# Kernel tuning notes

Measured on AMD Instinct MI355X. Metric: run time of the kernel, lower is better.

## Reference

```python
import jax, jax.numpy as jnp
import numpy as np


def _conv(x, w, b, pad):
    o = jax.lax.conv_general_dilated(x, w, (1, 1), [(pad, pad), (pad, pad)],
                                     dimension_numbers=('NCHW', 'OIHW', 'NCHW'))
    return o + b[None, :, None, None]


def _prelu(x, a):
    return jnp.where(x >= 0, x, a * x)


def _bn(x, g, b):
    # training-mode BatchNorm2d (biased variance, eps=1e-5)
    m = jnp.mean(x, axis=(0, 2, 3), keepdims=True)
    v = jnp.var(x, axis=(0, 2, 3), keepdims=True)
    return (x - m) * jax.lax.rsqrt(v + 1e-5) * g[None, :, None, None] + b[None, :, None, None]


def _maxpool2(x):
    return jax.lax.reduce_window(x, -jnp.inf, jax.lax.max, (1, 1, 2, 2), (1, 1, 2, 2), 'VALID')


def _up2(x):
    # bilinear upsample x2, align_corners=True
    B, C, H, W = x.shape
    Ho, Wo = 2 * H, 2 * W
    ys = jnp.arange(Ho, dtype=x.dtype) * ((H - 1) / (Ho - 1))
    xs = jnp.arange(Wo, dtype=x.dtype) * ((W - 1) / (Wo - 1))
    y0 = jnp.floor(ys).astype(jnp.int32)
    y1 = jnp.minimum(y0 + 1, H - 1)
    wy = (ys - y0.astype(x.dtype))[:, None]
    x0 = jnp.floor(xs).astype(jnp.int32)
    x1 = jnp.minimum(x0 + 1, W - 1)
    wx = xs - x0.astype(x.dtype)
    rows = x[:, :, y0, :] * (1 - wy) + x[:, :, y1, :] * wy  # [B,C,Ho,W]
    return rows[:, :, :, x0] * (1 - wx) + rows[:, :, :, x1] * wx


def _dyn_conv(x, w):
    # per-sample dynamic conv: x [B,1,H,W], w [B,Cout,k,k], pad = k//2 - 1
    # fused as a single grouped conv (groups = B) instead of B*Cout tiny launches
    B, Cout, k, _ = w.shape
    pad = k // 2 - 1
    xi = x.reshape(1, B, x.shape[2], x.shape[3])
    wi = w.reshape(B * Cout, 1, k, k)
    o = jax.lax.conv_general_dilated(xi, wi, (1, 1), [(pad, pad), (pad, pad)],
                                     dimension_numbers=('NCHW', 'OIHW', 'NCHW'),
                                     feature_group_count=B)
    return o.reshape(B, Cout, o.shape[2], o.shape[3])


def _double(x, w1, b1, w2, b2, a1, a2):
    return _prelu(_conv(_prelu(_conv(x, w1, b1, 1), a1), w2, b2, 1), a2)


def _forward(x, w, c1_w, c1_b, d2_w1, d2_b1, d2_w2, d2_b2, d3_w1, d3_b1, d3_w2, d3_b2,
             d4_w1, d4_b1, d4_w2, d4_b2, u3_w1, u3_b1, u3_w2, u3_b2, u2_w1, u2_b1,
             u2_w2, u2_b2, u1_w1, u1_b1, u1_w2, u1_b2, last_w, last_b,
             bn1_g, bn1_b, bn2_g, bn2_b, bn3_g, bn3_b, bn4_g, bn4_b, prelu_a):
    c1 = _prelu(_dyn_conv(x, w), prelu_a[0])          # [B,32,H-1,W-1]
    c1 = _prelu(_conv(c1, c1_w, c1_b, 2), prelu_a[1])  # 4x4 pad 2 -> [B,32,H,W]
    c1 = _bn(c1, bn1_g, bn1_b)
    h = _maxpool2(c1)
    c2 = _bn(_double(h, d2_w1, d2_b1, d2_w2, d2_b2, prelu_a[2], prelu_a[3]), bn2_g, bn2_b)
    h = _maxpool2(c2)
    c3 = _bn(_double(h, d3_w1, d3_b1, d3_w2, d3_b2, prelu_a[4], prelu_a[5]), bn3_g, bn3_b)
    h = _maxpool2(c3)
    h = _bn(_double(h, d4_w1, d4_b1, d4_w2, d4_b2, prelu_a[6], prelu_a[7]), bn4_g, bn4_b)
    h = jnp.concatenate([_up2(h), c3], axis=1)  # 512+256
    h = _double(h, u3_w1, u3_b1, u3_w2, u3_b2, prelu_a[8], prelu_a[9])
    h = jnp.concatenate([_up2(h), c2], axis=1)  # 256+128
    h = _double(h, u2_w1, u2_b1, u2_w2, u2_b2, prelu_a[10], prelu_a[11])
    h = jnp.concatenate([_up2(h), c1], axis=1)  # 128+32
    h = _double(h, u1_w1, u1_b1, u1_w2, u1_b2, prelu_a[12], prelu_a[13])
    return _conv(h, last_w, last_b, 0)


def setup_inputs() -> dict:
    key = jax.random.key(0)
    ks = iter(jax.random.split(key, 32))
    d = {}
    d['x'] = jax.random.normal(next(ks), (8, 1, 256, 256), jnp.float32)
    d['w'] = jax.random.normal(next(ks), (8, 32, 8, 8), jnp.float32) * 0.1
    wspecs = [('c1_w', (32, 32, 4, 4)), ('d2_w1', (128, 32, 3, 3)), ('d2_w2', (128, 128, 3, 3)),
              ('d3_w1', (256, 128, 3, 3)), ('d3_w2', (256, 256, 3, 3)),
              ('d4_w1', (512, 256, 3, 3)), ('d4_w2', (512, 512, 3, 3)),
              ('u3_w1', (256, 768, 3, 3)), ('u3_w2', (256, 256, 3, 3)),
              ('u2_w1', (128, 384, 3, 3)), ('u2_w2', (128, 128, 3, 3)),
              ('u1_w1', (32, 160, 3, 3)), ('u1_w2', (32, 32, 3, 3)), ('last_w', (1, 32, 1, 1))]
    for name, shp in wspecs:
        d[name] = jax.random.normal(next(ks), shp, jnp.float32) * 0.05
        d[name.replace('_w', '_b')] = jnp.zeros((shp[0],), jnp.float32)
    for name, c in [('bn1', 32), ('bn2', 128), ('bn3', 256), ('bn4', 512)]:
        d[name + '_g'] = jnp.ones((c,), jnp.float32)
        d[name + '_b'] = jnp.zeros((c,), jnp.float32)
    d['prelu_a'] = jnp.full((14,), 0.25, jnp.float32)
    return d


def reference(x, w, c1_w, c1_b, d2_w1, d2_b1, d2_w2, d2_b2, d3_w1, d3_b1, d3_w2, d3_b2,
              d4_w1, d4_b1, d4_w2, d4_b2, u3_w1, u3_b1, u3_w2, u3_b2, u2_w1, u2_b1,
              u2_w2, u2_b2, u1_w1, u1_b1, u1_w2, u1_b2, last_w, last_b,
              bn1_g, bn1_b, bn2_g, bn2_b, bn3_g, bn3_b, bn4_g, bn4_b, prelu_a):
    return _forward(x, w, c1_w, c1_b, d2_w1, d2_b1, d2_w2, d2_b2, d3_w1, d3_b1,
                    d3_w2, d3_b2, d4_w1, d4_b1, d4_w2, d4_b2, u3_w1, u3_b1, u3_w2,
                    u3_b2, u2_w1, u2_b1, u2_w2, u2_b2, u1_w1, u1_b1, u1_w2, u1_b2,
                    last_w, last_b, bn1_g, bn1_b, bn2_g, bn2_b, bn3_g, bn3_b,
                    bn4_g, bn4_b, prelu_a)
```

## Files before the change

kernel.cpp:

```cpp
#include <hip/hip_runtime.h>
#include <hip/hip_bf16.h>
#include <cstddef>


typedef _Float16 h16;
typedef __attribute__((ext_vector_type(8))) _Float16 h16x8;
typedef __attribute__((ext_vector_type(4))) float f32x4;
union F8 { uint4 u; h16x8 h; };
union UH { unsigned u; h16 h[2]; };

__device__ __forceinline__ float h2f(unsigned short s) {
    union { h16 h; unsigned short s; } c; c.s = s; return (float)c.h;
}
__device__ __forceinline__ unsigned short f2h(float f) {
    union { h16 h; unsigned short s; } c; c.h = (h16)f; return c.s;
}
__device__ __forceinline__ unsigned pack2(float a, float b) {
    return (unsigned)f2h(a) | ((unsigned)f2h(b) << 16);
}
__device__ __forceinline__ void up8(const uint4& v, float* f) {
    f[0]=h2f(v.x&0xffff); f[1]=h2f(v.x>>16);
    f[2]=h2f(v.y&0xffff); f[3]=h2f(v.y>>16);
    f[4]=h2f(v.z&0xffff); f[5]=h2f(v.z>>16);
    f[6]=h2f(v.w&0xffff); f[7]=h2f(v.w>>16);
}

__global__ void k_pack(const float* __restrict__ w, h16* __restrict__ pw,
                       int I, int T, int OB)
{
    int i8 = blockIdx.x * 64 + threadIdx.x;
    if (i8 >= (I >> 3)) return;
    int t = blockIdx.y, o = blockIdx.z;
    int ob = o / OB, om = o - ob * OB;
    int mt = om >> 4, m16 = om & 15;
    int chunk = i8 >> 2, quad = i8 & 3;
    int lane = quad * 16 + m16;
    int nch = I >> 5;
    size_t grp = ((((size_t)ob * T + t) * nch + chunk) * (OB >> 4) + mt) * 64 + lane;
    const float* src = w + ((size_t)o * I + i8 * 8) * T + t;
    h16* d = pw + grp * 8;
#pragma unroll
    for (int j = 0; j < 8; ++j) d[j] = (h16)src[(size_t)j * T];
}

template<int KH, int KW, int PAD, bool UPS, int MT>
__global__ __launch_bounds__(256, 2) void k_conv_mfma(
    const h16* __restrict__ src1, int C1n, int H1, int W1,
    const h16* __restrict__ src2, int C2n,
    int Hin, int Win, int Ho, int Wo,
    const h16* __restrict__ PW, const float* __restrict__ bias,
    const float* __restrict__ pa, int aidx,
    h16* __restrict__ out, int Cout)
{
    constexpr int WINH = 8 + KH - 1, WINW = 32 + KW - 1;
    constexpr int NPIX = WINH * WINW;
    constexpr int NIT  = NPIX * 4;
    constexpr int MAXIT = (NIT + 255) / 256;
    constexpr int TAPS = KH * KW;
    __shared__ unsigned short lds[2][NPIX * 36];

    const int tid = threadIdx.x;
    const int lane = tid & 63, wv = tid >> 6;
    const int quad = lane >> 4, m16 = lane & 15;
    const int nCb = Cout / (16 * MT);
    const int b  = blockIdx.z / nCb, cb = blockIdx.z % nCb;
    const int x0 = blockIdx.x * 32, y0 = blockIdx.y * 8;
    const int Cin = C1n + C2n;
    const int nch = Cin >> 5;
    const int co_base = cb * (16 * MT);
    const int srcH = UPS ? Hin : H1;
    const int srcW = UPS ? Win : W1;

    int lof[MAXIT];
    int g1[MAXIT];
    int fl[MAXIT];
    unsigned fyfx[MAXIT];
    int g2[MAXIT];

    const float ry = UPS ? (float)(H1 - 1) / (float)(Hin - 1) : 0.f;
    const float rx = UPS ? (float)(W1 - 1) / (float)(Win - 1) : 0.f;
    const int W1C = UPS ? W1 * C1n : 0;

#pragma unroll
    for (int it = 0; it < MAXIT; ++it) {
        int i = tid + it * 256;
        if (i >= NIT) { lof[it] = -1; g1[it] = -1; g2[it] = -1; fl[it] = 0; fyfx[it] = 0; continue; }
        int p = i >> 2, q = i & 3;
        int wy = p / WINW, wx = p - wy * WINW;
        int yy = y0 - PAD + wy, xx = x0 - PAD + wx;
        lof[it] = p * 36 + q * 8;
        bool val = (unsigned)yy < (unsigned)srcH && (unsigned)xx < (unsigned)srcW;
        if (UPS) {
            fl[it] = 0; fyfx[it] = 0; g1[it] = -1; g2[it] = -1;
            if (val) {
                float ys = yy * ry, xs = xx * rx;
                int yl0 = (int)ys, xl0 = (int)xs;
                float fy = ys - (float)yl0, fx = xs - (float)xl0;
                g1[it] = ((b * H1 + yl0) * W1 + xl0) * C1n + q * 8;
                fl[it] = (yl0 < H1 - 1 ? 1 : 0) | (xl0 < W1 - 1 ? 2 : 0);
                fyfx[it] = pack2(fy, fx);
                g2[it] = ((b * Hin + yy) * Win + xx) * C2n + q * 8;
            }
        } else {
            fl[it] = 0; fyfx[it] = 0; g2[it] = -1;
            g1[it] = val ? ((b * H1 + yy) * W1 + xx) * C1n + q * 8 : -1;
        }
    }

    f32x4 acc[MT][4];
#pragma unroll
    for (int i = 0; i < MT; ++i)
#pragma unroll
        for (int j = 0; j < 4; ++j) acc[i][j] = (f32x4){0.f, 0.f, 0.f, 0.f};

    auto stage = [&](int c0, unsigned short* buf) {
        if (UPS && c0 < C1n) {
#pragma unroll
            for (int it = 0; it < MAXIT; ++it) {
                int lo = lof[it];
                if (lo < 0) continue;
                uint2 lo8 = {0u, 0u}, hi8 = {0u, 0u};
                int g = g1[it];
                if (g >= 0) {
                    const h16* p00 = src1 + g + c0;
                    int oy = (fl[it] & 1) ? W1C : 0;
                    int ox = (fl[it] & 2) ? C1n : 0;
                    F8 v00, v01, v10, v11;
                    v00.u = *(const uint4*)(p00);
                    v01.u = *(const uint4*)(p00 + ox);
                    v10.u = *(const uint4*)(p00 + oy);
                    v11.u = *(const uint4*)(p00 + oy + ox);
                    UH t; t.u = fyfx[it];
                    h16 fy = t.h[0], fx = t.h[1];
                    h16x8 r0 = v00.h + (v10.h - v00.h) * fy;
                    h16x8 r1 = v01.h + (v11.h - v01.h) * fy;
                    F8 rr; rr.h = r0 + (r1 - r0) * fx;
                    lo8 = make_uint2(rr.u.x, rr.u.y);
                    hi8 = make_uint2(rr.u.z, rr.u.w);
                }
                *(uint2*)&buf[lo] = lo8;
                *(uint2*)&buf[lo + 4] = hi8;
            }
        } else if (UPS) {
            int cs = c0 - C1n;
#pragma unroll
            for (int it = 0; it < MAXIT; ++it) {
                int lo = lof[it];
                if (lo < 0) continue;
                uint4 v = {0u, 0u, 0u, 0u};
                int g = g2[it];
                if (g >= 0) v = *(const uint4*)(src2 + g + cs);
                *(uint2*)&buf[lo] = make_uint2(v.x, v.y);
                *(uint2*)&buf[lo + 4] = make_uint2(v.z, v.w);
            }
        } else {
#pragma unroll
            for (int it = 0; it < MAXIT; ++it) {
                int lo = lof[it];
                if (lo < 0) continue;
                uint4 v = {0u, 0u, 0u, 0u};
                int g = g1[it];
                if (g >= 0) v = *(const uint4*)(src1 + g + c0);
                *(uint2*)&buf[lo] = make_uint2(v.x, v.y);
                *(uint2*)&buf[lo + 4] = make_uint2(v.z, v.w);
            }
        }
    };

    const uint4* PW4 = (const uint4*)PW;
    auto sweep = [&](int ci, const unsigned short* buf) {
        size_t abase = (((size_t)cb * TAPS) * nch + ci) * (MT * 64) + lane;
        const size_t astep = (size_t)nch * (MT * 64);
#pragma unroll
        for (int ky = 0; ky < KH; ++ky) {
#pragma unroll
            for (int kx = 0; kx < KW; ++kx) {
                const int tap = ky * KW + kx;
                F8 a[MT];
#pragma unroll
                for (int mt = 0; mt < MT; ++mt)
                    a[mt].u = PW4[abase + (size_t)tap * astep + mt * 64];
#pragma unroll
                for (int nt = 0; nt < 4; ++nt) {
                    int rowl = (wv << 1) + (nt >> 1);
                    int col  = ((nt & 1) << 4) + m16;
                    int li = ((rowl + ky) * WINW + col + kx) * 36 + quad * 8;
                    F8 bf;
                    ((uint2*)&bf)[0] = *(const uint2*)&buf[li];
                    ((uint2*)&bf)[1] = *(const uint2*)&buf[li + 4];
#pragma unroll
                    for (int mt = 0; mt < MT; ++mt)
                        acc[mt][nt] = __builtin_amdgcn_mfma_f32_16x16x32_f16(
                            a[mt].h, bf.h, acc[mt][nt], 0, 0, 0);
                }
            }
        }
    };

    stage(0, lds[0]);
    __syncthreads();
    for (int ci = 0; ci < nch; ++ci) {
        int p = ci & 1;
        if (ci + 1 < nch) stage((ci + 1) << 5, lds[p ^ 1]);
        sweep(ci, lds[p]);
        __syncthreads();
    }

    const float alpha = pa[aidx];
#pragma unroll
    for (int mt = 0; mt < MT; ++mt) {
        int co = co_base + mt * 16 + quad * 4;
        float4 bi = *(const float4*)(bias + co);
#pragma unroll
        for (int nt = 0; nt < 4; ++nt) {
            int y = y0 + (wv << 1) + (nt >> 1);
            int x = x0 + ((nt & 1) << 4) + m16;
            float v0 = acc[mt][nt][0] + bi.x;
            float v1 = acc[mt][nt][1] + bi.y;
            float v2 = acc[mt][nt][2] + bi.z;
            float v3 = acc[mt][nt][3] + bi.w;
            v0 = v0 >= 0.f ? v0 : alpha * v0;
            v1 = v1 >= 0.f ? v1 : alpha * v1;
            v2 = v2 >= 0.f ? v2 : alpha * v2;
            v3 = v3 >= 0.f ? v3 : alpha * v3;
            uint2 r; r.x = pack2(v0, v1); r.y = pack2(v2, v3);
            *(uint2*)(out + ((size_t)((b * Ho + y) * Wo + x)) * Cout + co) = r;
        }
    }
}

__global__ __launch_bounds__(256) void k_dynconv(
    const float* __restrict__ x,
    const float* __restrict__ w,
    const float* __restrict__ pa,
    h16* __restrict__ out)
{
    __shared__ float wl[2048];
    int b = blockIdx.y;
    for (int j = threadIdx.x; j < 2048; j += 256) {
        int t = j >> 5, co = j & 31;
        wl[j] = w[((size_t)(b * 32 + co)) * 64 + t];
    }
    __syncthreads();
    int idx = blockIdx.x * 256 + threadIdx.x;
    if (idx >= 65025) return;
    int py = idx / 255, px = idx - py * 255;
    float acc[32];
#pragma unroll
    for (int c = 0; c < 32; ++c) acc[c] = 0.f;
    const float* xp = x + (size_t)b * 65536;
#pragma unroll
    for (int ky = 0; ky < 8; ++ky) {
        int iy = py + ky - 3;
        if ((unsigned)iy >= 256u) continue;
        const float* row = xp + iy * 256;
#pragma unroll
        for (int kx = 0; kx < 8; ++kx) {
            int ix = px + kx - 3;
            if ((unsigned)ix >= 256u) continue;
            float v = row[ix];
            const float4* wr = (const float4*)&wl[(ky * 8 + kx) * 32];
#pragma unroll
            for (int cg = 0; cg < 8; ++cg) {
                float4 wv = wr[cg];
                acc[cg*4+0] += v * wv.x; acc[cg*4+1] += v * wv.y;
                acc[cg*4+2] += v * wv.z; acc[cg*4+3] += v * wv.w;
            }
        }
    }
    float a = pa[0];
    h16* op = out + ((size_t)(b * 65025 + idx)) * 32;
#pragma unroll
    for (int cg = 0; cg < 4; ++cg) {
        float v[8];
#pragma unroll
        for (int k = 0; k < 8; ++k) {
            float t = acc[cg * 8 + k];
            v[k] = t >= 0.f ? t : a * t;
        }
        uint4 r;
        r.x = pack2(v[0], v[1]); r.y = pack2(v[2], v[3]);
        r.z = pack2(v[4], v[5]); r.w = pack2(v[6], v[7]);
        *(uint4*)(op + cg * 8) = r;
    }
}

__global__ __launch_bounds__(256) void k_pool(
    const h16* __restrict__ in, h16* __restrict__ out,
    int Hin, int Win, int C, int lc8, int lwo, int count)
{
    int idx = blockIdx.x * 256 + threadIdx.x;
    if (idx >= count) return;
    int b = blockIdx.y;
    int c8 = idx & ((1 << lc8) - 1);
    int t  = idx >> lc8;
    int ox = t & ((1 << lwo) - 1);
    int oy = t >> lwo;
    const h16* p = in + ((size_t)((b * Hin + oy * 2) * Win + ox * 2)) * C + c8 * 8;
    uint4 v00 = *(const uint4*)p;
    uint4 v01 = *(const uint4*)(p + C);
    uint4 v10 = *(const uint4*)(p + (size_t)Win * C);
    uint4 v11 = *(const uint4*)(p + (size_t)Win * C + C);
    float a[8], bb[8], c[8], d[8];
    up8(v00, a); up8(v01, bb); up8(v10, c); up8(v11, d);
    uint4 r;
    float m[8];
#pragma unroll
    for (int k = 0; k < 8; ++k) m[k] = fmaxf(fmaxf(a[k], bb[k]), fmaxf(c[k], d[k]));
    r.x = pack2(m[0], m[1]); r.y = pack2(m[2], m[3]);
    r.z = pack2(m[4], m[5]); r.w = pack2(m[6], m[7]);
    int Wo = 1 << lwo;
    *(uint4*)(out + ((size_t)((b * (Hin >> 1) + oy) * Wo + ox)) * C + c8 * 8) = r;
}

__global__ __launch_bounds__(256) void k_bnstats(
    const h16* __restrict__ x, int C, int N, float* __restrict__ sums)
{
    __shared__ float ls[1024];
    for (int j = threadIdx.x; j < 2 * C; j += 256) ls[j] = 0.f;
    __syncthreads();
    int start = blockIdx.x * 256 + threadIdx.x;
    int stride = gridDim.x * 256;
    int c = start & (C - 1);
    float s = 0.f, q = 0.f;
    for (int i = start; i < N; i += stride) {
        float v = h2f(((const unsigned short*)x)[i]);
        s += v; q += v * v;
    }
    atomicAdd(&ls[c], s);
    atomicAdd(&ls[C + c], q);
    __syncthreads();
    for (int j = threadIdx.x; j < 2 * C; j += 256) atomicAdd(&sums[j], ls[j]);
}

__global__ void k_bnfin(
    const float* __restrict__ sums, const float* __restrict__ g,
    const float* __restrict__ bta, int C, float invN, float* __restrict__ sc)
{
    int c = threadIdx.x;
    if (c >= C) return;
    float mean = sums[c] * invN;
    float var  = sums[C + c] * invN - mean * mean;
    float s    = g[c] / sqrtf(var + 1e-5f);
    sc[c]      = s;
    sc[C + c]  = bta[c] - mean * s;
}

__global__ __launch_bounds__(256) void k_bnapply(
    h16* __restrict__ x, int C, int N8, const float* __restrict__ sc)
{
    __shared__ float ls[1024];
    for (int j = threadIdx.x; j < 2 * C; j += 256) ls[j] = sc[j];
    __syncthreads();
    int idx = blockIdx.x * 256 + threadIdx.x;
    if (idx >= N8) return;
    int cb = (idx << 3) & (C - 1);
    h16* p = x + (size_t)idx * 8;
    uint4 v = *(const uint4*)p;
    float f[8];
    up8(v, f);
    uint4 r;
    float o[8];
#pragma unroll
    for (int k = 0; k < 8; ++k) o[k] = f[k] * ls[cb + k] + ls[C + cb + k];
    r.x = pack2(o[0], o[1]); r.y = pack2(o[2], o[3]);
    r.z = pack2(o[4], o[5]); r.w = pack2(o[6], o[7]);
    *(uint4*)p = r;
}

__global__ __launch_bounds__(256) void k_final(
    const h16* __restrict__ in, const float* __restrict__ w,
    const float* __restrict__ bias, float* __restrict__ out)
{
    int idx = blockIdx.x * 256 + threadIdx.x;
    if (idx >= 524288) return;
    const h16* p = in + (size_t)idx * 32;
    float acc = bias[0];
#pragma unroll
    for (int cg = 0; cg < 4; ++cg) {
        uint4 v = *(const uint4*)(p + cg * 8);
        float f[8];
        up8(v, f);
#pragma unroll
        for (int k = 0; k < 8; ++k) acc += f[k] * w[cg * 8 + k];
    }
    out[idx] = acc;
}

extern "C" void kernel_launch(void* const* d_in, const int* in_sizes, int n_in,
                              void* d_out, int out_size, void* d_ws, size_t ws_size,
                              hipStream_t stream)
{
    const float* x      = (const float*)d_in[0];
    const float* w      = (const float*)d_in[1];
    const float* c1_w   = (const float*)d_in[2];
    const float* c1_b   = (const float*)d_in[3];
    const float* d2_w1  = (const float*)d_in[4];
    const float* d2_b1  = (const float*)d_in[5];
    const float* d2_w2  = (const float*)d_in[6];
    const float* d2_b2  = (const float*)d_in[7];
    const float* d3_w1  = (const float*)d_in[8];
    const float* d3_b1  = (const float*)d_in[9];
    const float* d3_w2  = (const float*)d_in[10];
    const float* d3_b2  = (const float*)d_in[11];
    const float* d4_w1  = (const float*)d_in[12];
    const float* d4_b1  = (const float*)d_in[13];
    const float* d4_w2  = (const float*)d_in[14];
    const float* d4_b2  = (const float*)d_in[15];
    const float* u3_w1  = (const float*)d_in[16];
    const float* u3_b1  = (const float*)d_in[17];
    const float* u3_w2  = (const float*)d_in[18];
    const float* u3_b2  = (const float*)d_in[19];
    const float* u2_w1  = (const float*)d_in[20];
    const float* u2_b1  = (const float*)d_in[21];
    const float* u2_w2  = (const float*)d_in[22];
    const float* u2_b2  = (const float*)d_in[23];
    const float* u1_w1  = (const float*)d_in[24];
    const float* u1_b1  = (const float*)d_in[25];
    const float* u1_w2  = (const float*)d_in[26];
    const float* u1_b2  = (const float*)d_in[27];
    const float* last_w = (const float*)d_in[28];
    const float* last_b = (const float*)d_in[29];
    const float* bn1_g  = (const float*)d_in[30];
    const float* bn1_b  = (const float*)d_in[31];
    const float* bn2_g  = (const float*)d_in[32];
    const float* bn2_b  = (const float*)d_in[33];
    const float* bn3_g  = (const float*)d_in[34];
    const float* bn3_b  = (const float*)d_in[35];
    const float* bn4_g  = (const float*)d_in[36];
    const float* bn4_b  = (const float*)d_in[37];
    const float* pa     = (const float*)d_in[38];
    float* out = (float*)d_out;

    h16* A0 = (h16*)d_ws;
    h16* C1 = A0;
    h16* C2 = A0 + 16777216;
    h16* C3 = A0 + 33554432;
    h16* A  = A0 + 41943040;
    h16* B  = A0 + 58720256;
    h16* PWb= A0 + 75497472;
    float* SUMS = (float*)(A0 + 83126272);
    float* SC   = SUMS + 1024;
    size_t need = (size_t)83126272 * 2 + 8192;
    if (ws_size < need) return;

    h16* pw_c1   = PWb;
    h16* pw_d2w1 = PWb + 16384;
    h16* pw_d2w2 = PWb + 53248;
    h16* pw_d3w1 = PWb + 200704;
    h16* pw_d3w2 = PWb + 495616;
    h16* pw_d4w1 = PWb + 1085440;
    h16* pw_d4w2 = PWb + 2265088;
    h16* pw_u3w1 = PWb + 4624384;
    h16* pw_u3w2 = PWb + 6393856;
    h16* pw_u2w1 = PWb + 6983680;
    h16* pw_u2w2 = PWb + 7426048;
    h16* pw_u1w1 = PWb + 7573504;
    h16* pw_u1w2 = PWb + 7619584;

    dim3 blk(256);

    auto pack = [&](const float* src, h16* dst, int I, int T, int O, int OB) {
        k_pack<<<dim3(((I >> 3) + 63) / 64, T, O), 64, 0, stream>>>(src, dst, I, T, OB);
    };
    pack(c1_w,  pw_c1,   32, 16, 32, 32);
    pack(d2_w1, pw_d2w1, 32,  9, 128, 64);
    pack(d2_w2, pw_d2w2, 128, 9, 128, 64);
    pack(d3_w1, pw_d3w1, 128, 9, 256, 64);
    pack(d3_w2, pw_d3w2, 256, 9, 256, 64);
    pack(d4_w1, pw_d4w1, 256, 9, 512, 64);
    pack(d4_w2, pw_d4w2, 512, 9, 512, 64);
    pack(u3_w1, pw_u3w1, 768, 9, 256, 64);
    pack(u3_w2, pw_u3w2, 256, 9, 256, 64);
    pack(u2_w1, pw_u2w1, 384, 9, 128, 64);
    pack(u2_w2, pw_u2w2, 128, 9, 128, 64);
    pack(u1_w1, pw_u1w1, 160, 9, 32, 32);
    pack(u1_w2, pw_u1w2, 32,  9, 32, 32);

    auto bn = [&](h16* buf, int C, int N, const float* g, const float* bb) {
        hipMemsetAsync(SUMS, 0, 2 * C * sizeof(float), stream);
        k_bnstats<<<dim3(1024), blk, 0, stream>>>(buf, C, N, SUMS);
        k_bnfin<<<dim3(1), dim3(512), 0, stream>>>(SUMS, g, bb, C, (float)C / (float)N, SC);
        k_bnapply<<<dim3(N / 8 / 256), blk, 0, stream>>>(buf, C, N / 8, SC);
    };

    k_dynconv<<<dim3(255, 8), blk, 0, stream>>>(x, w, pa, A);
    k_conv_mfma<4,4,2,false,2><<<dim3(8, 32, 8), blk, 0, stream>>>(
        A, 32, 255, 255, nullptr, 0, 255, 255, 256, 256,
        pw_c1, c1_b, pa, 1, C1, 32);
    bn(C1, 32, 16777216, bn1_g, bn1_b);
    k_pool<<<dim3(256, 8), blk, 0, stream>>>(C1, B, 256, 256, 32, 2, 7, 65536);

    k_conv_mfma<3,3,1,false,4><<<dim3(4, 16, 16), blk, 0, stream>>>(
        B, 32, 128, 128, nullptr, 0, 128, 128, 128, 128,
        pw_d2w1, d2_b1, pa, 2, A, 128);
    k_conv_mfma<3,3,1,false,4><<<dim3(4, 16, 16), blk, 0, stream>>>(
        A, 128, 128, 128, nullptr, 0, 128, 128, 128, 128,
        pw_d2w2, d2_b2, pa, 3, C2, 128);
    bn(C2, 128, 16777216, bn2_g, bn2_b);
    k_pool<<<dim3(256, 8), blk, 0, stream>>>(C2, B, 128, 128, 128, 4, 6, 65536);

    k_conv_mfma<3,3,1,false,4><<<dim3(2, 8, 32), blk, 0, stream>>>(
        B, 128, 64, 64, nullptr, 0, 64, 64, 64, 64,
        pw_d3w1, d3_b1, pa, 4, A, 256);
    k_conv_mfma<3,3,1,false,4><<<dim3(2, 8, 32), blk, 0, stream>>>(
        A, 256, 64, 64, nullptr, 0, 64, 64, 64, 64,
        pw_d3w2, d3_b2, pa, 5, C3, 256);
    bn(C3, 256, 8388608, bn3_g, bn3_b);
    k_pool<<<dim3(128, 8), blk, 0, stream>>>(C3, B, 64, 64, 256, 5, 5, 32768);

    k_conv_mfma<3,3,1,false,4><<<dim3(1, 4, 64), blk, 0, stream>>>(
        B, 256, 32, 32, nullptr, 0, 32, 32, 32, 32,
        pw_d4w1, d4_b1, pa, 6, A, 512);
    k_conv_mfma<3,3,1,false,4><<<dim3(1, 4, 64), blk, 0, stream>>>(
        A, 512, 32, 32, nullptr, 0, 32, 32, 32, 32,
        pw_d4w2, d4_b2, pa, 7, B, 512);
    bn(B, 512, 4194304, bn4_g, bn4_b);

    k_conv_mfma<3,3,1,true,4><<<dim3(2, 8, 32), blk, 0, stream>>>(
        B, 512, 32, 32, C3, 256, 64, 64, 64, 64,
        pw_u3w1, u3_b1, pa, 8, A, 256);
    k_conv_mfma<3,3,1,false,4><<<dim3(2, 8, 32), blk, 0, stream>>>(
        A, 256, 64, 64, nullptr, 0, 64, 64, 64, 64,
        pw_u3w2, u3_b2, pa, 9, B, 256);

    k_conv_mfma<3,3,1,true,4><<<dim3(4, 16, 16), blk, 0, stream>>>(
        B, 256, 64, 64, C2, 128, 128, 128, 128, 128,
        pw_u2w1, u2_b1, pa, 10, A, 128);
    k_conv_mfma<3,3,1,false,4><<<dim3(4, 16, 16), blk, 0, stream>>>(
        A, 128, 128, 128, nullptr, 0, 128, 128, 128, 128,
        pw_u2w2, u2_b2, pa, 11, B, 128);

    k_conv_mfma<3,3,1,true,2><<<dim3(8, 32, 8), blk, 0, stream>>>(
        B, 128, 128, 128, C1, 32, 256, 256, 256, 256,
        pw_u1w1, u1_b1, pa, 12, A, 32);
    k_conv_mfma<3,3,1,false,2><<<dim3(8, 32, 8), blk, 0, stream>>>(
        A, 32, 256, 256, nullptr, 0, 256, 256, 256, 256,
        pw_u1w2, u1_b2, pa, 13, B, 32);

    k_final<<<dim3(2048), blk, 0, stream>>>(B, last_w, last_b, out);
}
```

Before: 1.255 ms.

## Compress per-thread staging state and raise conv kernel occupancy to three blocks

Per-thread precomputed staging arrays (LDS offset, flags, interpolation weights, skip-source offsets) are packed into a single bitfield word plus one global offset. Interpolation weights and skip addresses are now recomputed on the fly inside the staging loop. This frees registers so launch bounds can ask for three blocks per CU instead of two, giving more latency hiding. The cost is extra integer and float arithmetic in every channel-chunk stage and possible spills if the compiler cannot fit the tighter register budget.

```diff
diff --git a/kernel.cpp b/kernel.cpp
--- a/kernel.cpp
+++ b/kernel.cpp
@@ -7,7 +7,6 @@
 typedef __attribute__((ext_vector_type(8))) _Float16 h16x8;
 typedef __attribute__((ext_vector_type(4))) float f32x4;
 union F8 { uint4 u; h16x8 h; };
-union UH { unsigned u; h16 h[2]; };
 
 __device__ __forceinline__ float h2f(unsigned short s) {
     union { h16 h; unsigned short s; } c; c.s = s; return (float)c.h;
@@ -44,7 +43,7 @@
 }
 
 template<int KH, int KW, int PAD, bool UPS, int MT>
-__global__ __launch_bounds__(256, 2) void k_conv_mfma(
+__global__ __launch_bounds__(256, 3) void k_conv_mfma(
     const h16* __restrict__ src1, int C1n, int H1, int W1,
     const h16* __restrict__ src2, int C2n,
     int Hin, int Win, int Ho, int Wo,
@@ -71,39 +70,34 @@
     const int srcH = UPS ? Hin : H1;
     const int srcW = UPS ? Win : W1;
 
-    int lof[MAXIT];
-    int g1[MAXIT];
-    int fl[MAXIT];
-    unsigned fyfx[MAXIT];
-    int g2[MAXIT];
-
     const float ry = UPS ? (float)(H1 - 1) / (float)(Hin - 1) : 0.f;
     const float rx = UPS ? (float)(W1 - 1) / (float)(Win - 1) : 0.f;
     const int W1C = UPS ? W1 * C1n : 0;
 
+    int lofl[MAXIT];
+    int g1[MAXIT];
 #pragma unroll
     for (int it = 0; it < MAXIT; ++it) {
         int i = tid + it * 256;
-        if (i >= NIT) { lof[it] = -1; g1[it] = -1; g2[it] = -1; fl[it] = 0; fyfx[it] = 0; continue; }
+        if (i >= NIT) { lofl[it] = -1; g1[it] = -1; continue; }
         int p = i >> 2, q = i & 3;
         int wy = p / WINW, wx = p - wy * WINW;
         int yy = y0 - PAD + wy, xx = x0 - PAD + wx;
-        lof[it] = p * 36 + q * 8;
+        int lof = p * 36 + q * 8;
         bool val = (unsigned)yy < (unsigned)srcH && (unsigned)xx < (unsigned)srcW;
         if (UPS) {
-            fl[it] = 0; fyfx[it] = 0; g1[it] = -1; g2[it] = -1;
+            int fl = 0;
+            g1[it] = -1;
             if (val) {
                 float ys = yy * ry, xs = xx * rx;
                 int yl0 = (int)ys, xl0 = (int)xs;
-                float fy = ys - (float)yl0, fx = xs - (float)xl0;
                 g1[it] = ((b * H1 + yl0) * W1 + xl0) * C1n + q * 8;
-                fl[it] = (yl0 < H1 - 1 ? 1 : 0) | (xl0 < W1 - 1 ? 2 : 0);
-                fyfx[it] = pack2(fy, fx);
-                g2[it] = ((b * Hin + yy) * Win + xx) * C2n + q * 8;
+                fl = (yl0 < H1 - 1 ? 1 : 0) | (xl0 < W1 - 1 ? 2 : 0);
             }
+            lofl[it] = lof | (fl << 16) | (val ? (1 << 18) : 0);
         } else {
-            fl[it] = 0; fyfx[it] = 0; g2[it] = -1;
             g1[it] = val ? ((b * H1 + yy) * W1 + xx) * C1n + q * 8 : -1;
+            lofl[it] = lof;
         }
     }
 
@@ -117,21 +111,27 @@
         if (UPS && c0 < C1n) {
 #pragma unroll
             for (int it = 0; it < MAXIT; ++it) {
-                int lo = lof[it];
-                if (lo < 0) continue;
+                int e = lofl[it];
+                if (e < 0) continue;
+                int lo = e & 0xFFFF;
                 uint2 lo8 = {0u, 0u}, hi8 = {0u, 0u};
                 int g = g1[it];
                 if (g >= 0) {
+                    int i = tid + it * 256;
+                    int p = i >> 2;
+                    int wy = p / WINW, wx = p - wy * WINW;
+                    float ys = (y0 - PAD + wy) * ry;
+                    float xs = (x0 - PAD + wx) * rx;
+                    h16 fy = (h16)(ys - floorf(ys));
+                    h16 fx = (h16)(xs - floorf(xs));
                     const h16* p00 = src1 + g + c0;
-                    int oy = (fl[it] & 1) ? W1C : 0;
-                    int ox = (fl[it] & 2) ? C1n : 0;
+                    int oy = (e & (1 << 16)) ? W1C : 0;
+                    int ox = (e & (2 << 16)) ? C1n : 0;
                     F8 v00, v01, v10, v11;
                     v00.u = *(const uint4*)(p00);
                     v01.u = *(const uint4*)(p00 + ox);
                     v10.u = *(const uint4*)(p00 + oy);
                     v11.u = *(const uint4*)(p00 + oy + ox);
-                    UH t; t.u = fyfx[it];
-                    h16 fy = t.h[0], fx = t.h[1];
                     h16x8 r0 = v00.h + (v10.h - v00.h) * fy;
                     h16x8 r1 = v01.h + (v11.h - v01.h) * fy;
                     F8 rr; rr.h = r0 + (r1 - r0) * fx;
@@ -145,24 +145,30 @@
             int cs = c0 - C1n;
 #pragma unroll
             for (int it = 0; it < MAXIT; ++it) {
-                int lo = lof[it];
-                if (lo < 0) continue;
+                int e = lofl[it];
+                if (e < 0) continue;
+                int lo = e & 0xFFFF;
                 uint4 v = {0u, 0u, 0u, 0u};
-                int g = g2[it];
-                if (g >= 0) v = *(const uint4*)(src2 + g + cs);
+                if (e & (1 << 18)) {
+                    int i = tid + it * 256;
+                    int q = i & 3, p = i >> 2;
+                    int wy = p / WINW, wx = p - wy * WINW;
+                    int yy = y0 - PAD + wy, xx = x0 - PAD + wx;
+                    v = *(const uint4*)(src2 + ((b * Hin + yy) * Win + xx) * C2n + q * 8 + cs);
+                }
                 *(uint2*)&buf[lo] = make_uint2(v.x, v.y);
                 *(uint2*)&buf[lo + 4] = make_uint2(v.z, v.w);
             }
         } else {
 #pragma unroll
             for (int it = 0; it < MAXIT; ++it) {
-                int lo = lof[it];
-                if (lo < 0) continue;
+                int e = lofl[it];
+                if (e < 0) continue;
                 uint4 v = {0u, 0u, 0u, 0u};
                 int g = g1[it];
                 if (g >= 0) v = *(const uint4*)(src1 + g + c0);
-                *(uint2*)&buf[lo] = make_uint2(v.x, v.y);
-                *(uint2*)&buf[lo + 4] = make_uint2(v.z, v.w);
+                *(uint2*)&buf[e] = make_uint2(v.x, v.y);
+                *(uint2*)&buf[e + 4] = make_uint2(v.z, v.w);
             }
         }
     };
```

After: 1.583 ms. 26.1% more time.
